# Performance work log

Hardware: AMD Instinct MI355X
Metric: run time of the kernel (lower is better)

Reference implementation:

```python
import jax, jax.numpy as jnp
import numpy as np

NEG = -1e32
EPS_LN = 1e-5

def _layer_norm(x, w, b):
    mu = jnp.mean(x, axis=-1, keepdims=True)
    var = jnp.mean((x - mu) ** 2, axis=-1, keepdims=True)
    return (x - mu) / jnp.sqrt(var + EPS_LN) * w + b

def setup_inputs() -> dict:
    key = jax.random.key(0)
    ks = jax.random.split(key, 10)
    B, S, D, H, F = 2, 2048, 1024, 16, 4096
    s = 0.02
    return {
        "query": jax.random.normal(ks[0], (B, S, D), jnp.float32),
        "key": jax.random.normal(ks[1], (B, S, D), jnp.float32),
        "values": jax.random.normal(ks[2], (B, S, D), jnp.float32),
        "Wk": jax.random.normal(ks[3], (D, D), jnp.float32) * s,
        "bk": jnp.zeros((D,), jnp.float32),
        "Wv": jax.random.normal(ks[4], (D, D), jnp.float32) * s,
        "bv": jnp.zeros((D,), jnp.float32),
        "Wo": jax.random.normal(ks[5], (D, D), jnp.float32) * s,
        "bo": jnp.zeros((D,), jnp.float32),
        "gammas": jax.random.normal(ks[6], (H, 1, 1), jnp.float32),
        "ln1_w": jnp.ones((D,), jnp.float32),
        "ln1_b": jnp.zeros((D,), jnp.float32),
        "W1": jax.random.normal(ks[7], (F, D), jnp.float32) * s,
        "b1": jnp.zeros((F,), jnp.float32),
        "W2": jax.random.normal(ks[8], (D, F), jnp.float32) * s,
        "b2": jnp.zeros((D,), jnp.float32),
        "ln2_w": jnp.ones((D,), jnp.float32),
        "ln2_b": jnp.zeros((D,), jnp.float32),
        "mask": 1,
    }

def _forward(query, key, values, Wk, bk, Wv, bv, Wo, bo, gammas,
             ln1_w, ln1_b, W1, b1, W2, b2, ln2_w, ln2_b, mask):
    B, S, D = query.shape
    H = gammas.shape[0]
    dk = D // H
    # kq_same=True: q and k both use k_linear
    def proj(x, W, b):
        return (x @ W.T + b).reshape(B, S, H, dk).transpose(0, 2, 1, 3)  # bhsd
    q = proj(query, Wk, bk)
    k = proj(key, Wk, bk)
    v = proj(values, Wv, bv)

    scores = jnp.einsum("bhqd,bhkd->bhqk", q, k) / np.sqrt(dk).astype(np.float32)
    # src_mask: np.triu(ones, k=mask)==0 -> allowed where j <= i + mask - 1
    allow = jnp.tril(jnp.ones((S, S), bool), k=mask - 1)[None, None]  # (1,1,S,S)

    # --- distance decay (no_grad block in torch) ---
    scores_ = jax.nn.softmax(jnp.where(allow, scores, NEG), axis=-1)
    scores_ = scores_ * allow.astype(scores_.dtype)
    distcum = jnp.cumsum(scores_, axis=-1)
    disttotal = jnp.sum(scores_, axis=-1, keepdims=True)
    idx = jnp.arange(S)
    position_effect = jnp.abs(idx[:, None] - idx[None, :]).astype(jnp.float32)[None, None]
    dist_scores = jnp.sqrt(jnp.clip((disttotal - distcum) * position_effect, 0.0, None))
    gamma = -jax.nn.softplus(gammas)[None]  # (1,H,1,1)
    total_effect = jnp.clip(jnp.exp(dist_scores * gamma), 1e-5, 1e5)
    total_effect = jax.lax.stop_gradient(total_effect)
    # ---

    scores = scores * total_effect
    scores = jnp.where(allow, scores, NEG)
    attn = jax.nn.softmax(scores, axis=-1)
    out = jnp.einsum("bhqk,bhkd->bhqd", attn, v)
    concat = out.transpose(0, 2, 1, 3).reshape(B, S, D)
    query2 = concat @ Wo.T + bo

    x = _layer_norm(query + query2, ln1_w, ln1_b)
    ff = jax.nn.relu(x @ W1.T + b1) @ W2.T + b2
    x = _layer_norm(x + ff, ln2_w, ln2_b)
    return x

def reference(query, key, values, Wk, bk, Wv, bv, Wo, bo, gammas,
              ln1_w, ln1_b, W1, b1, W2, b2, ln2_w, ln2_b, mask):
    return _forward(query, key, values, Wk, bk, Wv, bv, Wo, bo, gammas,
                    ln1_w, ln1_b, W1, b1, W2, b2, ln2_w, ln2_b, mask)
```

## Files before the change

kernel.cpp:

```cpp
#include <hip/hip_runtime.h>
#include <hip/hip_bf16.h>

#define B_   2
#define S_   2048
#define D_   1024
#define H_   16
#define DK_  64
#define F_   4096
#define M_   (B_*S_)
#define PD   72

typedef __attribute__((ext_vector_type(8))) short short8;
typedef __attribute__((ext_vector_type(4))) float f32x4;

__device__ __forceinline__ float bf2f(unsigned short s) { return __uint_as_float(((unsigned int)s) << 16); }
__device__ __forceinline__ unsigned short f2bf(float f) {
    unsigned int u = __float_as_uint(f);
    u += 0x7fffu + ((u >> 16) & 1u);
    return (unsigned short)(u >> 16);
}

__device__ __forceinline__ bool probe_f32(const unsigned int* p) {
    return *p == 0x3F800000u;
}
__device__ __forceinline__ float ld1e(const void* p, size_t idx, bool f32) {
    return f32 ? ((const float*)p)[idx] : bf2f(((const unsigned short*)p)[idx]);
}
__device__ __forceinline__ void st1e(void* p, size_t idx, bool f32, float v) {
    if (f32) ((float*)p)[idx] = v;
    else     ((unsigned short*)p)[idx] = f2bf(v);
}

__device__ __forceinline__ void async16(void* lds, const void* g) {
    __builtin_amdgcn_global_load_lds(
        (const __attribute__((address_space(1))) void*)g,
        (__attribute__((address_space(3))) void*)lds, 16, 0, 0);
}

__device__ __forceinline__ unsigned int cvt_pk_bf16(float a, float b) {
    unsigned int r;
    asm("v_cvt_pk_bf16_f32 %0, %1, %2" : "=v"(r) : "v"(a), "v"(b));
    return r;
}

template <bool IS_MAX>
__device__ __forceinline__ float block_reduce(float val, float* buf, int tid) {
    buf[tid] = val;
    __syncthreads();
    #pragma unroll
    for (int off = 128; off > 0; off >>= 1) {
        if (tid < off) {
            float o = buf[tid + off];
            buf[tid] = IS_MAX ? fmaxf(buf[tid], o) : (buf[tid] + o);
        }
        __syncthreads();
    }
    float r = buf[0];
    __syncthreads();
    return r;
}

__global__ __launch_bounds__(256) void cvt_all(
    const void* __restrict__ W1, const void* __restrict__ W2,
    const void* __restrict__ Wk, const void* __restrict__ Wv,
    const void* __restrict__ Wo,
    const void* __restrict__ Qi, const void* __restrict__ Ki,
    const void* __restrict__ Vi,
    unsigned short* __restrict__ W1b, unsigned short* __restrict__ W2b,
    unsigned short* __restrict__ Wkb, unsigned short* __restrict__ Wvb,
    unsigned short* __restrict__ Wob,
    unsigned short* __restrict__ qcb, unsigned short* __restrict__ kcb,
    unsigned short* __restrict__ vcb,
    const unsigned int* __restrict__ probe)
{
    const bool p32 = probe_f32(probe);
    const int blk = blockIdx.x;
    const void* src;
    unsigned short* dst;
    int off;
    if (blk < 2048)      { src = W1; dst = W1b; off = blk; }
    else if (blk < 4096) { src = W2; dst = W2b; off = blk - 2048; }
    else if (blk < 4608) { src = Wk; dst = Wkb; off = blk - 4096; }
    else if (blk < 5120) { src = Wv; dst = Wvb; off = blk - 4608; }
    else if (blk < 5632) { src = Wo; dst = Wob; off = blk - 5120; }
    else if (blk < 7680) { if (!p32) return; src = Qi; dst = qcb; off = blk - 5632; }
    else if (blk < 9728) { if (!p32) return; src = Ki; dst = kcb; off = blk - 7680; }
    else                 { if (!p32) return; src = Vi; dst = vcb; off = blk - 9728; }
    const int i8 = (off * 256 + threadIdx.x) * 8;
    if (p32) {
        const float4 a = *(const float4*)((const float*)src + i8);
        const float4 b = *(const float4*)((const float*)src + i8 + 4);
        short8 o;
        o[0] = (short)f2bf(a.x); o[1] = (short)f2bf(a.y);
        o[2] = (short)f2bf(a.z); o[3] = (short)f2bf(a.w);
        o[4] = (short)f2bf(b.x); o[5] = (short)f2bf(b.y);
        o[6] = (short)f2bf(b.z); o[7] = (short)f2bf(b.w);
        *(short8*)(dst + i8) = o;
    } else {
        *(uint4*)(dst + i8) = *(const uint4*)((const unsigned short*)src + i8);
    }
}

template <int RELU, int AEXT, int CEXT>
__device__ __forceinline__ void gemm_body(
    const void* __restrict__ A,
    const unsigned short* __restrict__ W,
    const void* __restrict__ bias,
    void* __restrict__ C,
    int M, int N, int K, bool p32, int bx, int by)
{
    __shared__ unsigned short As[2][128 * 32];
    __shared__ unsigned short Ws[2][128 * 32];

    const bool a32 = AEXT && p32;
    const bool c32 = CEXT && p32;

    const int tid = threadIdx.x;
    const int lane = tid & 63;
    const int w = tid >> 6;
    const int wr = w >> 1;
    const int wc = w & 1;
    const int col16 = lane & 15;
    const int quad = lane >> 4;

    const int m0 = by * 128;
    const int n0 = bx * 128;

    const int c0 = tid, c1 = 256 + tid;
    const int r0 = c0 >> 2, kc0 = (c0 & 3) * 8;
    const int r1 = c1 >> 2, kc1 = (c1 & 3) * 8;

    f32x4 acc[4][4];
    #pragma unroll
    for (int mt = 0; mt < 4; mt++)
        #pragma unroll
        for (int nt = 0; nt < 4; nt++)
            acc[mt][nt] = (f32x4){0.f, 0.f, 0.f, 0.f};

    auto stage = [&](int bb, int k0) {
        async16(&Ws[bb][c0 * 8], W + (size_t)(n0 + r0) * K + k0 + kc0);
        async16(&Ws[bb][c1 * 8], W + (size_t)(n0 + r1) * K + k0 + kc1);
        if (a32) {
            const float* a0 = (const float*)A + (size_t)(m0 + r0) * K + k0 + kc0;
            const float* a1 = (const float*)A + (size_t)(m0 + r1) * K + k0 + kc1;
            const float4 x0 = *(const float4*)a0, y0 = *(const float4*)(a0 + 4);
            const float4 x1 = *(const float4*)a1, y1 = *(const float4*)(a1 + 4);
            short8 s0, s1;
            s0[0] = (short)f2bf(x0.x); s0[1] = (short)f2bf(x0.y);
            s0[2] = (short)f2bf(x0.z); s0[3] = (short)f2bf(x0.w);
            s0[4] = (short)f2bf(y0.x); s0[5] = (short)f2bf(y0.y);
            s0[6] = (short)f2bf(y0.z); s0[7] = (short)f2bf(y0.w);
            s1[0] = (short)f2bf(x1.x); s1[1] = (short)f2bf(x1.y);
            s1[2] = (short)f2bf(x1.z); s1[3] = (short)f2bf(x1.w);
            s1[4] = (short)f2bf(y1.x); s1[5] = (short)f2bf(y1.y);
            s1[6] = (short)f2bf(y1.z); s1[7] = (short)f2bf(y1.w);
            *(short8*)&As[bb][c0 * 8] = s0;
            *(short8*)&As[bb][c1 * 8] = s1;
        } else {
            const unsigned short* Ab = (const unsigned short*)A;
            async16(&As[bb][c0 * 8], Ab + (size_t)(m0 + r0) * K + k0 + kc0);
            async16(&As[bb][c1 * 8], Ab + (size_t)(m0 + r1) * K + k0 + kc1);
        }
    };

    stage(0, 0);
    __syncthreads();
    int cur = 0;
    for (int k0 = 0; k0 < K; k0 += 32) {
        const int nxt = cur ^ 1;
        if (k0 + 32 < K) stage(nxt, k0 + 32);

        short8 av[4], bv[4];
        #pragma unroll
        for (int mt = 0; mt < 4; mt++)
            av[mt] = *(const short8*)&As[cur][(wr * 64 + mt * 16 + col16) * 32 + quad * 8];
        #pragma unroll
        for (int nt = 0; nt < 4; nt++)
            bv[nt] = *(const short8*)&Ws[cur][(wc * 64 + nt * 16 + col16) * 32 + quad * 8];
        #pragma unroll
        for (int mt = 0; mt < 4; mt++)
            #pragma unroll
            for (int nt = 0; nt < 4; nt++)
                acc[mt][nt] = __builtin_amdgcn_mfma_f32_16x16x32_bf16(
                    av[mt], bv[nt], acc[mt][nt], 0, 0, 0);
        __syncthreads();
        cur = nxt;
    }

    #pragma unroll
    for (int mt = 0; mt < 4; mt++) {
        const int row = m0 + wr * 64 + mt * 16 + quad * 4;
        #pragma unroll
        for (int nt = 0; nt < 4; nt++) {
            const int col = n0 + wc * 64 + nt * 16 + col16;
            const float bb = ld1e(bias, col, p32);
            #pragma unroll
            for (int r = 0; r < 4; r++) {
                float v = acc[mt][nt][r] + bb;
                if (RELU) v = fmaxf(v, 0.f);
                st1e(C, (size_t)(row + r) * N + col, c32, v);
            }
        }
    }
}

template <int RELU, int AEXT, int CEXT>
__global__ __launch_bounds__(256) void gemm_mf(
    const void* __restrict__ A,
    const unsigned short* __restrict__ W,
    const void* __restrict__ bias,
    void* __restrict__ C,
    int M, int N, int K,
    const unsigned int* __restrict__ probe)
{
    gemm_body<RELU, AEXT, CEXT>(A, W, bias, C, M, N, K, probe_f32(probe),
                                blockIdx.x, blockIdx.y);
}

template <int RELU, int CEXT>
__global__ __launch_bounds__(512) void gemm_sk(
    const unsigned short* __restrict__ A,
    const unsigned short* __restrict__ W,
    const void* __restrict__ bias,
    void* __restrict__ C,
    int M, int N, int K,
    const unsigned int* __restrict__ probe)
{
    __shared__ unsigned short SS[2][2][2][128 * 32];
    float* const R = (float*)&SS[0][0][0][0];

    const bool p32 = probe_f32(probe);
    const bool c32 = CEXT && p32;

    const int tid = threadIdx.x;
    const int g = tid >> 8;
    const int tl = tid & 255;
    const int lane = tl & 63;
    const int w = tl >> 6;
    const int wr = w >> 1;
    const int wc = w & 1;
    const int col16 = lane & 15;
    const int quad = lane >> 4;

    const int m0 = blockIdx.y * 128;
    const int n0 = blockIdx.x * 128;

    const int c0 = tl, c1 = 256 + tl;
    const int r0 = c0 >> 2, kc0 = (c0 & 3) * 8;
    const int r1 = c1 >> 2, kc1 = (c1 & 3) * 8;

    const int Kh = K >> 1;
    const int kbeg = g * Kh;

    f32x4 acc[4][4];
    #pragma unroll
    for (int mt = 0; mt < 4; mt++)
        #pragma unroll
        for (int nt = 0; nt < 4; nt++)
            acc[mt][nt] = (f32x4){0.f, 0.f, 0.f, 0.f};

    auto stage = [&](int bb, int k0) {
        async16(&SS[g][bb][1][c0 * 8], W + (size_t)(n0 + r0) * K + k0 + kc0);
        async16(&SS[g][bb][1][c1 * 8], W + (size_t)(n0 + r1) * K + k0 + kc1);
        async16(&SS[g][bb][0][c0 * 8], A + (size_t)(m0 + r0) * K + k0 + kc0);
        async16(&SS[g][bb][0][c1 * 8], A + (size_t)(m0 + r1) * K + k0 + kc1);
    };

    stage(0, kbeg);
    __syncthreads();
    int cur = 0;
    for (int kk = 0; kk < Kh; kk += 32) {
        const int nxt = cur ^ 1;
        if (kk + 32 < Kh) stage(nxt, kbeg + kk + 32);

        short8 av[4], bv[4];
        #pragma unroll
        for (int mt = 0; mt < 4; mt++)
            av[mt] = *(const short8*)&SS[g][cur][0][(wr * 64 + mt * 16 + col16) * 32 + quad * 8];
        #pragma unroll
        for (int nt = 0; nt < 4; nt++)
            bv[nt] = *(const short8*)&SS[g][cur][1][(wc * 64 + nt * 16 + col16) * 32 + quad * 8];
        #pragma unroll
        for (int mt = 0; mt < 4; mt++)
            #pragma unroll
            for (int nt = 0; nt < 4; nt++)
                acc[mt][nt] = __builtin_amdgcn_mfma_f32_16x16x32_bf16(
                    av[mt], bv[nt], acc[mt][nt], 0, 0, 0);
        __syncthreads();
        cur = nxt;
    }

    __syncthreads();
    if (g == 1) {
        #pragma unroll
        for (int mt = 0; mt < 4; mt++)
            #pragma unroll
            for (int nt = 0; nt < 4; nt++) {
                const int lrow = wr * 64 + mt * 16 + quad * 4;
                const int lcol = wc * 64 + nt * 16 + col16;
                #pragma unroll
                for (int r = 0; r < 4; r++)
                    R[(lrow + r) * 128 + lcol] = acc[mt][nt][r];
            }
    }
    __syncthreads();
    if (g == 0) {
        #pragma unroll
        for (int mt = 0; mt < 4; mt++) {
            const int lrow = wr * 64 + mt * 16 + quad * 4;
            const int row = m0 + lrow;
            #pragma unroll
            for (int nt = 0; nt < 4; nt++) {
                const int lcol = wc * 64 + nt * 16 + col16;
                const int col = n0 + lcol;
                const float bb = ld1e(bias, col, p32);
                #pragma unroll
                for (int r = 0; r < 4; r++) {
                    float v = acc[mt][nt][r] + R[(lrow + r) * 128 + lcol] + bb;
                    if (RELU) v = fmaxf(v, 0.f);
                    st1e(C, (size_t)(row + r) * N + col, c32, v);
                }
            }
        }
    }
}

__global__ __launch_bounds__(256) void gemm_proj(
    const void* __restrict__ q_orig, const void* __restrict__ k_orig,
    const void* __restrict__ v_orig,
    const unsigned short* __restrict__ qcb, const unsigned short* __restrict__ kcb,
    const unsigned short* __restrict__ vcb,
    const unsigned short* __restrict__ Wkb, const unsigned short* __restrict__ Wvb,
    const void* __restrict__ bk, const void* __restrict__ bv,
    unsigned short* __restrict__ qw, unsigned short* __restrict__ kw,
    unsigned short* __restrict__ vw,
    const unsigned int* __restrict__ probe)
{
    const bool p32 = probe_f32(probe);
    const int z = blockIdx.z;
    const unsigned short* W = (z == 2) ? Wvb : Wkb;
    const void* bias = (z == 2) ? bv : bk;
    void* C = (z == 0) ? (void*)qw : (z == 1) ? (void*)kw : (void*)vw;
    if (z == 2 && p32 && vcb == nullptr) {
        gemm_body<0, 1, 0>(v_orig, W, bias, C, M_, D_, D_, p32,
                           blockIdx.x, blockIdx.y);
    } else {
        const void* A = (z == 0) ? (p32 ? (const void*)qcb : q_orig)
                      : (z == 1) ? (p32 ? (const void*)kcb : k_orig)
                                 : (p32 ? (const void*)vcb : v_orig);
        gemm_body<0, 0, 0>(A, W, bias, C, M_, D_, D_, p32,
                           blockIdx.x, blockIdx.y);
    }
}

__global__ __launch_bounds__(256) void vtrans(
    const unsigned short* __restrict__ vw,
    unsigned short* __restrict__ vtg)
{
    __shared__ unsigned short T[64 * PD];
    const int tid = threadIdx.x;
    const int bid = blockIdx.x;
    const int bh = bid & 31;
    const int kt = bid >> 5;
    const int h = bh & 15, b = bh >> 4;
    #pragma unroll
    for (int cc = 0; cc < 2; cc++) {
        const int c = tid + cc * 256;
        const int key = c >> 3, dc = c & 7;
        const uint4 u = *(const uint4*)(vw + (size_t)(b * S_ + kt * 64 + key) * D_ + h * 64 + dc * 8);
        unsigned short* dst = &T[(dc * 8) * PD + key];
        dst[0 * PD] = (unsigned short)(u.x & 0xffff);
        dst[1 * PD] = (unsigned short)(u.x >> 16);
        dst[2 * PD] = (unsigned short)(u.y & 0xffff);
        dst[3 * PD] = (unsigned short)(u.y >> 16);
        dst[4 * PD] = (unsigned short)(u.z & 0xffff);
        dst[5 * PD] = (unsigned short)(u.z >> 16);
        dst[6 * PD] = (unsigned short)(u.w & 0xffff);
        dst[7 * PD] = (unsigned short)(u.w >> 16);
    }
    __syncthreads();
    #pragma unroll
    for (int cc = 0; cc < 2; cc++) {
        const int c = tid + cc * 256;
        const int d = c >> 3, kc = c & 7;
        const uint4 u = *(const uint4*)&T[d * PD + kc * 8];
        *(uint4*)(vtg + ((size_t)bh * 64 + d) * S_ + kt * 64 + kc * 8) = u;
    }
}

__global__ __launch_bounds__(256) void attn_mfma(
    const unsigned short* __restrict__ qw,
    const unsigned short* __restrict__ kw,
    const unsigned short* __restrict__ vtg,
    const void* __restrict__ gam,
    const int* __restrict__ maskp,
    unsigned short* __restrict__ outc,
    const unsigned int* __restrict__ probe)
{
    __shared__ unsigned short Qs[64 * PD];
    __shared__ unsigned short Ks[64 * PD];
    __shared__ unsigned short Vt[64 * PD];
    __shared__ float ctS[64 * 33];
    __shared__ float rT1S[64];
    unsigned int* const Pu = (unsigned int*)Qs;

    const bool p32 = probe_f32(probe);
    const int tid = threadIdx.x;
    const int lane = tid & 63;
    const int w = tid >> 6;
    const int col16 = lane & 15;
    const int quad = lane >> 4;
    const int bid = blockIdx.x;
    const int qt = 31 - (bid >> 5);
    const int bh = bid & 31;
    const int h = bh & 15;
    const int b = bh >> 4;
    const int i0 = qt * 64;

    const int mask = *maskp;
    long long nje = (long long)i0 + 63 + (long long)mask;
    int njmax = (nje > S_) ? S_ : (int)nje;
    if (njmax < 1) njmax = 1;
    const int ntiles = (njmax + 63) >> 6;
    long long fm = (long long)i0 + (long long)mask - 64;
    int nfull = 0;
    if (fm >= 0) {
        long long v = (fm >> 6) + 1;
        nfull = (v > ntiles) ? ntiles : (int)v;
    }

    const float L2E = 1.44269504088896f;
    const float gval = ld1e(gam, h, p32);
    const float sp = (gval > 20.f) ? gval : log1pf(__expf(gval));
    const float g2 = -sp * L2E;
    const float SC2 = 0.125f * L2E;

    const int myrow = i0 + w * 16 + col16;
    const int limq = myrow + mask - quad * 4;

    #pragma unroll
    for (int cc = 0; cc < 2; cc++) {
        const int c = tid + cc * 256;
        const int row = c >> 3, dc = c & 7;
        const uint4 u = *(const uint4*)(qw + (size_t)(b * S_ + i0 + row) * D_ + h * 64 + dc * 8);
        *(uint4*)&Qs[row * PD + dc * 8] = u;
    }
    __syncthreads();

    short8 avq[2];
    #pragma unroll
    for (int ks = 0; ks < 2; ks++)
        avq[ks] = *(const short8*)&Qs[(w * 16 + col16) * PD + ks * 32 + quad * 8];

    for (int t = 0; t < ntiles; t++) {
        const int j0 = t * 64;
        __syncthreads();
        #pragma unroll
        for (int cc = 0; cc < 2; cc++) {
            const int c = tid + cc * 256;
            const int row = c >> 3, dc = c & 7;
            const uint4 u = *(const uint4*)(kw + (size_t)(b * S_ + j0 + row) * D_ + h * 64 + dc * 8);
            *(uint4*)&Ks[row * PD + dc * 8] = u;
        }
        __syncthreads();

        f32x4 acc[4];
        #pragma unroll
        for (int nt = 0; nt < 4; nt++) acc[nt] = (f32x4){0.f, 0.f, 0.f, 0.f};
        #pragma unroll
        for (int ks = 0; ks < 2; ks++)
            #pragma unroll
            for (int nt = 0; nt < 4; nt++) {
                const short8 kv = *(const short8*)&Ks[(nt * 16 + col16) * PD + ks * 32 + quad * 8];
                acc[nt] = __builtin_amdgcn_mfma_f32_16x16x32_bf16(kv, avq[ks], acc[nt], 0, 0, 0);
            }

        if (t >= nfull) {
            #pragma unroll
            for (int nt = 0; nt < 4; nt++) {
                const int Ln = limq - j0 - nt * 16;
                #pragma unroll
                for (int r = 0; r < 4; r++)
                    acc[nt][r] = (r < Ln) ? acc[nt][r] : -3.0e38f;
            }
        }

        float cs = 0.f;
        #pragma unroll
        for (int nt = 0; nt < 4; nt++)
            #pragma unroll
            for (int r = 0; r < 4; r++)
                cs += __builtin_amdgcn_exp2f(acc[nt][r] * SC2);
        cs += __shfl_xor(cs, 16, 64);
        cs += __shfl_xor(cs, 32, 64);

        if (lane < 16)
            ctS[(w * 16 + lane) * 33 + t] = cs;
    }

    __syncthreads();
    if (lane < 16) {
        const int row = w * 16 + lane;
        float runv = 0.f;
        for (int t = 0; t < ntiles; t++) {
            const float e = ctS[row * 33 + t];
            ctS[row * 33 + t] = runv;
            runv += e;
        }
        rT1S[row] = 1.0f / runv;
    }
    __syncthreads();

    const float rT1 = rT1S[w * 16 + col16];

    float l2 = 0.f;
    f32x4 O[4];
    #pragma unroll
    for (int nt = 0; nt < 4; nt++) O[nt] = (f32x4){0.f, 0.f, 0.f, 0.f};

    for (int t = 0; t < ntiles; t++) {
        const int j0 = t * 64;
        __syncthreads();
        #pragma unroll
        for (int cc = 0; cc < 2; cc++) {
            const int c = tid + cc * 256;
            const int row = c >> 3, dc = c & 7;
            const uint4 u = *(const uint4*)(kw + (size_t)(b * S_ + j0 + row) * D_ + h * 64 + dc * 8);
            *(uint4*)&Ks[row * PD + dc * 8] = u;
        }
        #pragma unroll
        for (int cc = 0; cc < 2; cc++) {
            const int c = tid + cc * 256;
            const int d = c >> 3, kc = c & 7;
            const uint4 u = *(const uint4*)(vtg + ((size_t)bh * 64 + d) * S_ + j0 + kc * 8);
            *(uint4*)&Vt[d * PD + kc * 8] = u;
        }
        __syncthreads();

        f32x4 acc[4];
        #pragma unroll
        for (int nt = 0; nt < 4; nt++) acc[nt] = (f32x4){0.f, 0.f, 0.f, 0.f};
        #pragma unroll
        for (int ks = 0; ks < 2; ks++)
            #pragma unroll
            for (int nt = 0; nt < 4; nt++) {
                const short8 kv = *(const short8*)&Ks[(nt * 16 + col16) * PD + ks * 32 + quad * 8];
                acc[nt] = __builtin_amdgcn_mfma_f32_16x16x32_bf16(kv, avq[ks], acc[nt], 0, 0, 0);
            }

        if (t >= nfull) {
            #pragma unroll
            for (int nt = 0; nt < 4; nt++) {
                const int Ln = limq - j0 - nt * 16;
                #pragma unroll
                for (int r = 0; r < 4; r++)
                    acc[nt][r] = (r < Ln) ? acc[nt][r] : -3.0e38f;
            }
        }

        float s2v[4][4], loc[4][4], run4[4];
        #pragma unroll
        for (int nt = 0; nt < 4; nt++) {
            float rr = 0.f;
            #pragma unroll
            for (int r = 0; r < 4; r++) {
                const float s2 = acc[nt][r] * SC2;
                s2v[nt][r] = s2;
                rr += __builtin_amdgcn_exp2f(s2);
                loc[nt][r] = rr;
            }
            run4[nt] = rr;
        }
        float excl[4], tot[4];
        #pragma unroll
        for (int nt = 0; nt < 4; nt++) {
            float v = run4[nt];
            const float u1 = __shfl_up(v, 16, 64); if (quad >= 1) v += u1;
            const float u2 = __shfl_up(v, 32, 64); if (quad >= 2) v += u2;
            excl[nt] = v - run4[nt];
            tot[nt] = __shfl(v, col16 + 48, 64);
        }

        const float pref = ctS[(w * 16 + col16) * 33 + t];
        float Cb = pref;
        #pragma unroll
        for (int nt = 0; nt < 4; nt++) {
            const float CeR = (Cb + excl[nt]) * rT1;
            const float d0f = (float)(myrow - j0 - nt * 16 - quad * 4);
            float p4[4];
            #pragma unroll
            for (int r = 0; r < 4; r++) {
                const float cumn = __builtin_fmaf(loc[nt][r], rT1, CeR);
                const float rem = fmaxf(1.f - cumn, 0.f);
                const float pe = fabsf(d0f - (float)r);
                const float te = fmaxf(
                    __builtin_amdgcn_exp2f(g2 * __builtin_amdgcn_sqrtf(rem * pe)), 1e-5f);
                const float tv = s2v[nt][r] * te;
                p4[r] = __builtin_amdgcn_exp2f(tv);
                l2 += p4[r];
            }
            uint2 pk;
            pk.x = cvt_pk_bf16(p4[0], p4[1]);
            pk.y = cvt_pk_bf16(p4[2], p4[3]);
            *(uint2*)&Pu[(w * 16 + col16) * 36 + nt * 8 + quad * 2] = pk;
            Cb += tot[nt];
        }

        const short8 pa0 = *(const short8*)&Pu[(w * 16 + col16) * 36 + 0 * 16 + quad * 4];
        const short8 pa1 = *(const short8*)&Pu[(w * 16 + col16) * 36 + 1 * 16 + quad * 4];
        #pragma unroll
        for (int nt = 0; nt < 4; nt++) {
            const short8 bv0 = *(const short8*)&Vt[(nt * 16 + col16) * PD + 0 * 32 + quad * 8];
            const short8 bv1 = *(const short8*)&Vt[(nt * 16 + col16) * PD + 1 * 32 + quad * 8];
            O[nt] = __builtin_amdgcn_mfma_f32_16x16x32_bf16(pa0, bv0, O[nt], 0, 0, 0);
            O[nt] = __builtin_amdgcn_mfma_f32_16x16x32_bf16(pa1, bv1, O[nt], 0, 0, 0);
        }
    }

    l2 += __shfl_xor(l2, 16, 64);
    l2 += __shfl_xor(l2, 32, 64);
    const float rl2 = 1.0f / l2;
    float rl2O[4];
    #pragma unroll
    for (int r = 0; r < 4; r++) rl2O[r] = __shfl(rl2, quad * 4 + r, 64);
    #pragma unroll
    for (int nt = 0; nt < 4; nt++)
        #pragma unroll
        for (int r = 0; r < 4; r++)
            outc[(size_t)(b * S_ + i0 + w * 16 + quad * 4 + r) * D_ + h * 64 + nt * 16 + col16] =
                f2bf(O[nt][r] * rl2O[r]);
}

__global__ __launch_bounds__(256) void ln_fused(
    const void* __restrict__ A,
    const void* __restrict__ Bq,
    const void* __restrict__ w,
    const void* __restrict__ bias,
    void* __restrict__ out,
    const unsigned int* __restrict__ probe, int aext, int bext, int oext)
{
    __shared__ float xs[D_];
    __shared__ float red[256];
    const bool p32 = probe_f32(probe);
    const bool a32 = aext && p32;
    const bool b32 = bext && p32;
    const bool o32 = oext && p32;

    const int tid = threadIdx.x;
    const size_t row = (size_t)blockIdx.x * D_;

    float lsum = 0.f;
    #pragma unroll
    for (int qq = 0; qq < 4; qq++) {
        const int j = tid + qq * 256;
        const float x = ld1e(A, row + j, a32) + ld1e(Bq, row + j, b32);
        xs[j] = x;
        lsum += x;
    }
    const float mu = block_reduce<false>(lsum, red, tid) * (1.0f / D_);

    float lv = 0.f;
    #pragma unroll
    for (int qq = 0; qq < 4; qq++) {
        const int j = tid + qq * 256;
        const float dd = xs[j] - mu;
        lv += dd * dd;
    }
    const float var = block_reduce<false>(lv, red, tid) * (1.0f / D_);
    const float rs = rsqrtf(var + 1e-5f);

    #pragma unroll
    for (int qq = 0; qq < 4; qq++) {
        const int j = tid + qq * 256;
        const float o = (xs[j] - mu) * rs * ld1e(w, j, p32) + ld1e(bias, j, p32);
        st1e(out, row + j, o32, o);
    }
}

extern "C" void kernel_launch(void* const* d_in, const int* in_sizes, int n_in,
                              void* d_out, int out_size, void* d_ws, size_t ws_size,
                              hipStream_t stream)
{
    (void)in_sizes; (void)n_in; (void)out_size;

    const void* query  = d_in[0];
    const void* key_   = d_in[1];
    const void* values = d_in[2];
    const void* Wk     = d_in[3];
    const void* bk     = d_in[4];
    const void* Wv     = d_in[5];
    const void* bv     = d_in[6];
    const void* Wo     = d_in[7];
    const void* bo     = d_in[8];
    const void* gammas = d_in[9];
    const void* ln1w   = d_in[10];
    const void* ln1b   = d_in[11];
    const void* W1     = d_in[12];
    const void* b1     = d_in[13];
    const void* W2     = d_in[14];
    const void* b2     = d_in[15];
    const void* ln2w   = d_in[16];
    const void* ln2b   = d_in[17];
    const int*  maskp  = (const int*)d_in[18];
    const unsigned int* probe = (const unsigned int*)ln1w;

    char* ws = (char*)d_ws;
    const size_t MiB = 1024 * 1024;
    unsigned short* W1b = (unsigned short*)(ws + 0 * MiB);
    unsigned short* W2b = (unsigned short*)(ws + 8 * MiB);
    unsigned short* Wkb = (unsigned short*)(ws + 16 * MiB);
    unsigned short* Wvb = (unsigned short*)(ws + 18 * MiB);
    unsigned short* Wob = (unsigned short*)(ws + 20 * MiB);
    unsigned short* qw  = (unsigned short*)(ws + 22 * MiB);
    unsigned short* kw  = (unsigned short*)(ws + 30 * MiB);
    unsigned short* vw  = (unsigned short*)(ws + 38 * MiB);
    unsigned short* cw  = (unsigned short*)(ws + 46 * MiB);
    unsigned short* vtg = (unsigned short*)(ws + 54 * MiB);
    unsigned short* x1  = (unsigned short*)(ws + 22 * MiB);
    unsigned short* fh  = (unsigned short*)(ws + 30 * MiB);
    unsigned short* qc  = (unsigned short*)(ws + 46 * MiB);
    unsigned short* kc  = (unsigned short*)(ws + 54 * MiB);
    unsigned short* vc  = (ws_size >= (size_t)70 * MiB)
                          ? (unsigned short*)(ws + 62 * MiB) : nullptr;

    const dim3 blk(256);
    const dim3 blk5(512);
    const int cvtgrid = vc ? 11776 : 9728;
    cvt_all<<<dim3(cvtgrid), blk, 0, stream>>>(
        W1, W2, Wk, Wv, Wo, query, key_, values,
        W1b, W2b, Wkb, Wvb, Wob, qc, kc, vc, probe);
    gemm_proj<<<dim3(D_ / 128, M_ / 128, 3), blk, 0, stream>>>(
        query, key_, values, qc, kc, vc, Wkb, Wvb, bk, bv, qw, kw, vw, probe);
    vtrans<<<dim3(1024), blk, 0, stream>>>(vw, vtg);
    attn_mfma<<<dim3(B_ * H_ * (S_ / 64)), blk, 0, stream>>>(
        qw, kw, vtg, gammas, maskp, cw, probe);
    gemm_sk<0, 0><<<dim3(D_ / 128, M_ / 128), blk5, 0, stream>>>(
        cw, Wob, bo, x1, M_, D_, D_, probe);
    ln_fused<<<dim3(M_), blk, 0, stream>>>(query, x1, ln1w, ln1b, x1, probe, 1, 0, 0);
    gemm_mf<1, 0, 0><<<dim3(F_ / 128, M_ / 128), blk, 0, stream>>>(
        x1, W1b, b1, fh, M_, F_, D_, probe);
    gemm_sk<0, 1><<<dim3(D_ / 128, M_ / 128), blk5, 0, stream>>>(
        fh, W2b, b2, d_out, M_, D_, F_, probe);
    ln_fused<<<dim3(M_), blk, 0, stream>>>(x1, d_out, ln2w, ln2b, d_out, probe, 0, 1, 1);
}
```

Measured before the change: 453.0 us.

## Swizzle GEMM LDS tiles, remap workgroups across XCDs, vectorize LayerNorm

Applies an XOR swizzle to the 16-byte chunk column used when staging A/W tiles into LDS and reading MFMA fragments, to reduce LDS bank conflicts in both GEMM kernels. Adds an XCD-aware remapping of the workgroup index so neighbouring tiles land on the same XCD and share L2. Rewrites the LayerNorm kernel to keep each thread's four contiguous elements in registers with vectorized loads and stores instead of a shared-memory row buffer. The remap assumes the grid size divides by 8 and that the swizzle matches on write and read; otherwise tiles could be misassigned or misread.

After: 446.8 us (median of 2 runs). No clear change (-1.4%).

```diff
diff --git a/kernel.cpp b/kernel.cpp
--- a/kernel.cpp
+++ b/kernel.cpp
@@ -41,6 +41,15 @@
     unsigned int r;
     asm("v_cvt_pk_bf16_f32 %0, %1, %2" : "=v"(r) : "v"(a), "v"(b));
     return r;
+}
+
+__device__ __forceinline__ void xcd_remap(int& bx, int& by) {
+    const int gx = gridDim.x, gy = gridDim.y;
+    const int nwg = gx * gy;
+    const int orig = by * gx + bx;
+    const int neo = (orig & 7) * (nwg >> 3) + (orig >> 3);
+    bx = neo / gy;
+    by = neo % gy;
 }
 
 template <bool IS_MAX>
@@ -127,8 +136,10 @@
     const int n0 = bx * 128;
 
     const int c0 = tid, c1 = 256 + tid;
-    const int r0 = c0 >> 2, kc0 = (c0 & 3) * 8;
-    const int r1 = c1 >> 2, kc1 = (c1 & 3) * 8;
+    const int r0 = c0 >> 2, kc0 = (((c0 & 3) ^ ((c0 >> 3) & 3)) * 8);
+    const int r1 = c1 >> 2, kc1 = (((c1 & 3) ^ ((c1 >> 3) & 3)) * 8);
+
+    const int fcol = ((quad ^ ((col16 >> 1) & 3)) * 8);
 
     f32x4 acc[4][4];
     #pragma unroll
@@ -173,10 +184,10 @@
         short8 av[4], bv[4];
         #pragma unroll
         for (int mt = 0; mt < 4; mt++)
-            av[mt] = *(const short8*)&As[cur][(wr * 64 + mt * 16 + col16) * 32 + quad * 8];
+            av[mt] = *(const short8*)&As[cur][(wr * 64 + mt * 16 + col16) * 32 + fcol];
         #pragma unroll
         for (int nt = 0; nt < 4; nt++)
-            bv[nt] = *(const short8*)&Ws[cur][(wc * 64 + nt * 16 + col16) * 32 + quad * 8];
+            bv[nt] = *(const short8*)&Ws[cur][(wc * 64 + nt * 16 + col16) * 32 + fcol];
         #pragma unroll
         for (int mt = 0; mt < 4; mt++)
             #pragma unroll
@@ -213,8 +224,9 @@
     int M, int N, int K,
     const unsigned int* __restrict__ probe)
 {
-    gemm_body<RELU, AEXT, CEXT>(A, W, bias, C, M, N, K, probe_f32(probe),
-                                blockIdx.x, blockIdx.y);
+    int bx = blockIdx.x, by = blockIdx.y;
+    xcd_remap(bx, by);
+    gemm_body<RELU, AEXT, CEXT>(A, W, bias, C, M, N, K, probe_f32(probe), bx, by);
 }
 
 template <int RELU, int CEXT>
@@ -242,12 +254,15 @@
     const int col16 = lane & 15;
     const int quad = lane >> 4;
 
-    const int m0 = blockIdx.y * 128;
-    const int n0 = blockIdx.x * 128;
+    int bx = blockIdx.x, by = blockIdx.y;
+    xcd_remap(bx, by);
+    const int m0 = by * 128;
+    const int n0 = bx * 128;
 
     const int c0 = tl, c1 = 256 + tl;
-    const int r0 = c0 >> 2, kc0 = (c0 & 3) * 8;
-    const int r1 = c1 >> 2, kc1 = (c1 & 3) * 8;
+    const int r0 = c0 >> 2, kc0 = (((c0 & 3) ^ ((c0 >> 3) & 3)) * 8);
+    const int r1 = c1 >> 2, kc1 = (((c1 & 3) ^ ((c1 >> 3) & 3)) * 8);
+    const int fcol = ((quad ^ ((col16 >> 1) & 3)) * 8);
 
     const int Kh = K >> 1;
     const int kbeg = g * Kh;
@@ -276,10 +291,10 @@
         short8 av[4], bv[4];
         #pragma unroll
         for (int mt = 0; mt < 4; mt++)
-            av[mt] = *(const short8*)&SS[g][cur][0][(wr * 64 + mt * 16 + col16) * 32 + quad * 8];
+            av[mt] = *(const short8*)&SS[g][cur][0][(wr * 64 + mt * 16 + col16) * 32 + fcol];
         #pragma unroll
         for (int nt = 0; nt < 4; nt++)
-            bv[nt] = *(const short8*)&SS[g][cur][1][(wc * 64 + nt * 16 + col16) * 32 + quad * 8];
+            bv[nt] = *(const short8*)&SS[g][cur][1][(wc * 64 + nt * 16 + col16) * 32 + fcol];
         #pragma unroll
         for (int mt = 0; mt < 4; mt++)
             #pragma unroll
@@ -639,7 +654,6 @@
     void* __restrict__ out,
     const unsigned int* __restrict__ probe, int aext, int bext, int oext)
 {
-    __shared__ float xs[D_];
     __shared__ float red[256];
     const bool p32 = probe_f32(probe);
     const bool a32 = aext && p32;
@@ -648,32 +662,68 @@
 
     const int tid = threadIdx.x;
     const size_t row = (size_t)blockIdx.x * D_;
+    const int j4 = tid * 4;
+
+    float xa[4], xb[4];
+    if (a32) {
+        const float4 t = *(const float4*)((const float*)A + row + j4);
+        xa[0] = t.x; xa[1] = t.y; xa[2] = t.z; xa[3] = t.w;
+    } else {
+        const ushort4 t = *(const ushort4*)((const unsigned short*)A + row + j4);
+        xa[0] = bf2f(t.x); xa[1] = bf2f(t.y); xa[2] = bf2f(t.z); xa[3] = bf2f(t.w);
+    }
+    if (b32) {
+        const float4 t = *(const float4*)((const float*)Bq + row + j4);
+        xb[0] = t.x; xb[1] = t.y; xb[2] = t.z; xb[3] = t.w;
+    } else {
+        const ushort4 t = *(const ushort4*)((const unsigned short*)Bq + row + j4);
+        xb[0] = bf2f(t.x); xb[1] = bf2f(t.y); xb[2] = bf2f(t.z); xb[3] = bf2f(t.w);
+    }
 
     float lsum = 0.f;
-    #pragma unroll
-    for (int qq = 0; qq < 4; qq++) {
-        const int j = tid + qq * 256;
-        const float x = ld1e(A, row + j, a32) + ld1e(Bq, row + j, b32);
-        xs[j] = x;
-        lsum += x;
+    float x4[4];
+    #pragma unroll
+    for (int k = 0; k < 4; k++) {
+        x4[k] = xa[k] + xb[k];
+        lsum += x4[k];
     }
     const float mu = block_reduce<false>(lsum, red, tid) * (1.0f / D_);
 
     float lv = 0.f;
     #pragma unroll
-    for (int qq = 0; qq < 4; qq++) {
-        const int j = tid + qq * 256;
-        const float dd = xs[j] - mu;
+    for (int k = 0; k < 4; k++) {
+        const float dd = x4[k] - mu;
         lv += dd * dd;
     }
     const float var = block_reduce<false>(lv, red, tid) * (1.0f / D_);
     const float rs = rsqrtf(var + 1e-5f);
 
-    #pragma unroll
-    for (int qq = 0; qq < 4; qq++) {
-        const int j = tid + qq * 256;
-        const float o = (xs[j] - mu) * rs * ld1e(w, j, p32) + ld1e(bias, j, p32);
-        st1e(out, row + j, o32, o);
+    float wv[4], bv[4];
+    if (p32) {
+        const float4 tw = *(const float4*)((const float*)w + j4);
+        const float4 tb = *(const float4*)((const float*)bias + j4);
+        wv[0] = tw.x; wv[1] = tw.y; wv[2] = tw.z; wv[3] = tw.w;
+        bv[0] = tb.x; bv[1] = tb.y; bv[2] = tb.z; bv[3] = tb.w;
+    } else {
+        const ushort4 tw = *(const ushort4*)((const unsigned short*)w + j4);
+        const ushort4 tb = *(const ushort4*)((const unsigned short*)bias + j4);
+        wv[0] = bf2f(tw.x); wv[1] = bf2f(tw.y); wv[2] = bf2f(tw.z); wv[3] = bf2f(tw.w);
+        bv[0] = bf2f(tb.x); bv[1] = bf2f(tb.y); bv[2] = bf2f(tb.z); bv[3] = bf2f(tb.w);
+    }
+
+    float o4[4];
+    #pragma unroll
+    for (int k = 0; k < 4; k++)
+        o4[k] = (x4[k] - mu) * rs * wv[k] + bv[k];
+
+    if (o32) {
+        float4 o; o.x = o4[0]; o.y = o4[1]; o.z = o4[2]; o.w = o4[3];
+        *(float4*)((float*)out + row + j4) = o;
+    } else {
+        uint2 pk;
+        pk.x = cvt_pk_bf16(o4[0], o4[1]);
+        pk.y = cvt_pk_bf16(o4[2], o4[3]);
+        *(uint2*)((unsigned short*)out + row + j4) = pk;
     }
 }
 
```
